# Performance work log

Hardware: AMD Instinct MI355X
Metric: run time of the kernel (lower is better)

The kernel has to match this reference:

```python
import jax, jax.numpy as jnp
import numpy as np

B = 131072
D_IN = 385          # 384-d embedding + 1 correctness feature
D_H = 192           # both trunk layers resolve to max(.,192)=192 per source
Q = 1000            # number of questions
C = 16              # classes per head (uniform padding of per-question heads)


def setup_inputs() -> dict:
    key = jax.random.key(0)
    ks = jax.random.split(key, 9)
    x = jax.random.normal(ks[0], (B, D_IN), dtype=jnp.float32)
    question_ids = jax.random.randint(ks[1], (B,), 0, Q, dtype=jnp.int32)
    is_correct = jax.random.randint(ks[2], (B,), 0, 2, dtype=jnp.int32)
    W1 = jax.random.normal(ks[3], (D_IN, D_H), dtype=jnp.float32) * 0.05
    b1 = jnp.zeros((D_H,), dtype=jnp.float32)
    W2 = jax.random.normal(ks[4], (D_H, D_H), dtype=jnp.float32) * 0.05
    b2 = jnp.zeros((D_H,), dtype=jnp.float32)
    # Head bank: slots [0,Q) = false heads, [Q,2Q) = true heads.
    W_heads = jax.random.normal(ks[5], (2 * Q, C, D_H), dtype=jnp.float32) * 0.05
    b_heads = jax.random.normal(ks[6], (2 * Q, C), dtype=jnp.float32) * 0.05
    return {"x": x, "question_ids": question_ids, "is_correct": is_correct,
            "W1": W1, "b1": b1, "W2": W2, "b2": b2,
            "W_heads": W_heads, "b_heads": b_heads}


def reference(x, question_ids, is_correct, W1, b1, W2, b2, W_heads, b_heads):
    # Shared trunk (eval mode: dropout = identity)
    h = jax.nn.relu(x @ W1 + b1)            # [B, 192]
    feat = jax.nn.relu(h @ W2 + b2)         # [B, 192]
    # Hard routing: pick true or false head for this question.
    Qn = W_heads.shape[0] // 2
    idx = question_ids + is_correct * Qn    # [B]
    Wq = W_heads[idx]                       # [B, C, 192] gather (memory-bound)
    bq = b_heads[idx]                       # [B, C]
    logits = jnp.einsum('bcd,bd->bc', Wq, feat) + bq  # per-sample routed linear
    return logits
```

## Files before the change

### kernel.cpp

```cpp
#include <hip/hip_runtime.h>
#include <hip/hip_bf16.h>
#include <stdint.h>
#include <stddef.h>


typedef short s8v __attribute__((ext_vector_type(8)));
typedef float f4v __attribute__((ext_vector_type(4)));
typedef float f4a __attribute__((ext_vector_type(4), aligned(4)));

typedef const void __attribute__((address_space(1))) *gas1_t;
typedef void __attribute__((address_space(3))) *las3_t;

namespace {
constexpr int kDin = 385;
constexpr int kDh  = 192;
constexpr int kQ   = 1000;
constexpr int kC   = 16;
constexpr int BM   = 64;
constexpr int NT   = 512;
constexpr int NK1  = 13;
constexpr int NK2  = 6;
constexpr int CHUNK = 12 * 64 * 8;
constexpr int H2   = 200;

constexpr size_t WS_W1   = 0;
constexpr size_t WS_W2   = 163840;
constexpr size_t WS_HIST = 245760;
constexpr size_t WS_CUR  = 253952;
constexpr size_t WS_PERM = 262144;

constexpr size_t WB_FEAT = 0;
constexpr size_t WB_W1   = 50331648;
constexpr size_t WB_W2   = WB_W1 + 159744;
constexpr size_t WB_HIST = WB_W2 + 73728;
constexpr size_t WB_CUR  = WB_HIST + 8192;
constexpr size_t WB_PERM = WB_CUR + 8192;
constexpr size_t WB_NEED = WB_PERM + 524288;
constexpr size_t WS_SANE_MAX = (1ull << 36);
}

__device__ __forceinline__ unsigned short f2bf(float f) {
  unsigned int u = __float_as_uint(f);
  u = u + 0x7fffu + ((u >> 16) & 1u);
  return (unsigned short)(u >> 16);
}

__device__ __forceinline__ unsigned int pk2(float lo, float hi) {
  union { __hip_bfloat162 h2; unsigned int u; } cv;
  cv.h2 = __float22bfloat162_rn(make_float2(lo, hi));
  return cv.u;
}

union s8u { s8v s; unsigned int u[4]; };

__device__ __forceinline__ void swz_one(const float* W, int K, int i,
                                        unsigned short* out) {
  int k = i / kDh;
  int c = i - k * kDh;
  float v = (k < K) ? W[(size_t)k * kDh + c] : 0.f;
  int oi = (k >> 5) * CHUNK + (((c >> 4) * 64 + ((k >> 3) & 3) * 16 + (c & 15)) << 3)
         + (k & 7);
  out[oi] = f2bf(v);
}

__global__ void combo_prep(const int* __restrict__ qid, const int* __restrict__ isc,
                           int B, int nbH,
                           const float* __restrict__ W1, const float* __restrict__ W2,
                           int* __restrict__ hist,
                           unsigned short* __restrict__ W1sw,
                           unsigned short* __restrict__ W2sw) {
  int bid = blockIdx.x;
  if (bid < nbH) {
    int i = bid * 256 + threadIdx.x;
    if (i < B) atomicAdd(&hist[qid[i] + isc[i] * kQ], 1);
  } else if (bid < nbH + 312) {
    swz_one(W1, kDin, (bid - nbH) * 256 + threadIdx.x, W1sw);
  } else {
    swz_one(W2, kDh, (bid - nbH - 312) * 256 + threadIdx.x, W2sw);
  }
}

__global__ __launch_bounds__(256)
void scatter2(const int* __restrict__ qid, const int* __restrict__ isc, int B,
              const int* __restrict__ hist, int* __restrict__ rank_ctr,
              int* __restrict__ perm) {
  __shared__ int sh[2048];
  __shared__ int ssum[256];
  int t = threadIdx.x;
  int4 a = ((const int4*)hist)[t * 2];
  int4 b = ((const int4*)hist)[t * 2 + 1];
  int s1 = a.x + a.y, s2 = s1 + a.z, s3 = s2 + a.w;
  int s4 = s3 + b.x, s5 = s4 + b.y, s6 = s5 + b.z, s7 = s6 + b.w;
  ssum[t] = s7;
  __syncthreads();
  #pragma unroll
  for (int d = 1; d < 256; d <<= 1) {
    int xv = (t >= d) ? ssum[t - d] : 0;
    __syncthreads();
    ssum[t] += xv;
    __syncthreads();
  }
  int base = ssum[t] - s7;
  sh[t * 8 + 0] = base;
  sh[t * 8 + 1] = base + a.x;
  sh[t * 8 + 2] = base + s1;
  sh[t * 8 + 3] = base + s2;
  sh[t * 8 + 4] = base + s3;
  sh[t * 8 + 5] = base + s4;
  sh[t * 8 + 6] = base + s5;
  sh[t * 8 + 7] = base + s6;
  __syncthreads();
  int i = blockIdx.x * 256 + t;
  if (i < B) {
    int h = qid[i] + isc[i] * kQ;
    int pos = sh[h] + atomicAdd(&rank_ctr[h], 1);
    perm[pos] = i;
  }
}

__global__ __launch_bounds__(NT, 8)
void trunk_k(const float* __restrict__ x,
             const float* __restrict__ b1,
             const float* __restrict__ b2,
             const unsigned short* __restrict__ W1sw,
             const unsigned short* __restrict__ W2sw,
             unsigned short* __restrict__ featG) {
  __shared__ __align__(16) unsigned short hS[BM * H2];
  __shared__ __align__(16) unsigned short bS[CHUNK];

  const int tid  = threadIdx.x;
  const int lane = tid & 63, wid = tid >> 6;
  const int m = lane & 15, quad = lane >> 4;
  const int rh = wid >> 1, ch = wid & 1;
  const int row0 = blockIdx.x * BM;

  {
    const char* g = (const char*)W1sw + (size_t)tid * 16;
    char* l = (char*)bS + ((tid >> 6) << 10);
    __builtin_amdgcn_global_load_lds((gas1_t)g, (las3_t)l, 16, 0, 0);
    if (tid < 256)
      __builtin_amdgcn_global_load_lds((gas1_t)(g + 8192), (las3_t)(l + 8192),
                                       16, 0, 0);
  }

  const float* px = x + (size_t)(row0 + rh * 16 + m) * kDin;

  f4v acc[6];
  #pragma unroll
  for (int t = 0; t < 6; ++t) acc[t] = (f4v){0.f, 0.f, 0.f, 0.f};

  f4a c0 = *(const f4a*)(px + quad * 8);
  f4a c1 = *(const f4a*)(px + quad * 8 + 4);
  float tl = 0.f;
  __syncthreads();

  #pragma unroll
  for (int kk = 0; kk < NK1; ++kk) {
    s8v a;
    if (kk < NK1 - 1) {
      s8u ua;
      ua.u[0] = pk2(c0[0], c0[1]); ua.u[1] = pk2(c0[2], c0[3]);
      ua.u[2] = pk2(c1[0], c1[1]); ua.u[3] = pk2(c1[2], c1[3]);
      a = ua.s;
    } else {
      a = (s8v){0,0,0,0,0,0,0,0};
      a[0] = (short)f2bf(tl);
    }

    #pragma unroll
    for (int t = 0; t < 6; ++t) {
      s8v b = *(const s8v*)&bS[((ch * 6 + t) * 64 + lane) * 8];
      acc[t] = __builtin_amdgcn_mfma_f32_16x16x32_bf16(a, b, acc[t], 0, 0, 0);
    }
    __syncthreads();

    {
      const unsigned short* np = (kk < NK1 - 1)
          ? W1sw + (size_t)(kk + 1) * CHUNK : W2sw;
      const char* g = (const char*)np + (size_t)tid * 16;
      char* l = (char*)bS + ((tid >> 6) << 10);
      __builtin_amdgcn_global_load_lds((gas1_t)g, (las3_t)l, 16, 0, 0);
      if (tid < 256)
        __builtin_amdgcn_global_load_lds((gas1_t)(g + 8192), (las3_t)(l + 8192),
                                         16, 0, 0);
    }
    if (kk < NK1 - 2) {
      c0 = *(const f4a*)(px + (kk + 1) * 32 + quad * 8);
      c1 = *(const f4a*)(px + (kk + 1) * 32 + quad * 8 + 4);
    } else if (kk == NK1 - 2) {
      tl = (quad == 0) ? px[384] : 0.f;
    }
    if (kk == NK1 - 1) {
      #pragma unroll
      for (int t = 0; t < 6; ++t) {
        int c = ch * 96 + t * 16 + m;
        float bb = b1[c];
        #pragma unroll
        for (int r4 = 0; r4 < 4; ++r4) {
          int r = rh * 16 + quad * 4 + r4;
          float v0 = acc[t][r4] + bb;
          hS[r * H2 + c] = f2bf(v0 > 0.f ? v0 : 0.f);
          acc[t][r4] = 0.f;
        }
      }
    }
    __syncthreads();
  }

  const int ar0 = (rh * 16 + m) * H2;
  #pragma unroll
  for (int k2 = 0; k2 < NK2; ++k2) {
    s8v a = *(const s8v*)&hS[ar0 + k2 * 32 + quad * 8];
    #pragma unroll
    for (int t = 0; t < 6; ++t) {
      s8v b = *(const s8v*)&bS[((ch * 6 + t) * 64 + lane) * 8];
      acc[t] = __builtin_amdgcn_mfma_f32_16x16x32_bf16(a, b, acc[t], 0, 0, 0);
    }
    __syncthreads();
    if (k2 < NK2 - 1) {
      const char* g = (const char*)(W2sw + (size_t)(k2 + 1) * CHUNK)
                    + (size_t)tid * 16;
      char* l = (char*)bS + ((tid >> 6) << 10);
      __builtin_amdgcn_global_load_lds((gas1_t)g, (las3_t)l, 16, 0, 0);
      if (tid < 256)
        __builtin_amdgcn_global_load_lds((gas1_t)(g + 8192), (las3_t)(l + 8192),
                                         16, 0, 0);
    } else {
      #pragma unroll
      for (int t = 0; t < 6; ++t) {
        int c = ch * 96 + t * 16 + m;
        float bb = b2[c];
        #pragma unroll
        for (int r4 = 0; r4 < 4; ++r4) {
          int r = rh * 16 + quad * 4 + r4;
          float v0 = acc[t][r4] + bb;
          hS[r * H2 + c] = f2bf(v0 > 0.f ? v0 : 0.f);
        }
      }
    }
    __syncthreads();
  }

  #pragma unroll
  for (int j = 0; j < 3; ++j) {
    int e = tid + j * NT;
    int row = e / 24, c8 = e - row * 24;
    *(s8v*)&featG[(size_t)(row0 + row) * kDh + c8 * 8] =
        *(const s8v*)&hS[row * H2 + c8 * 8];
  }
}

__global__ __launch_bounds__(NT, 8)
void head_k(const int* __restrict__ qid, const int* __restrict__ isc,
            const float* __restrict__ Wh, const float* __restrict__ bh,
            const unsigned short* __restrict__ featG,
            const int* __restrict__ perm, float* __restrict__ out) {
  __shared__ int permS[BM];
  __shared__ int idxS[BM];

  const int tid  = threadIdx.x;
  const int lane = tid & 63, wid = tid >> 6;
  const int m = lane & 15, quad = lane >> 4;
  const int rh = wid >> 1, ch = wid & 1;
  const int row0 = blockIdx.x * BM;

  if (tid < BM) {
    int p = perm[row0 + tid];
    permS[tid] = p;
    idxS[tid] = qid[p] + isc[p] * kQ;
  }
  __syncthreads();

  const int w16 = rh * 16;
  const unsigned short* fp = featG + (size_t)permS[w16 + m] * kDh + quad * 8;
  s8v f[6];
  #pragma unroll
  for (int kk = 0; kk < 6; ++kk) f[kk] = *(const s8v*)(fp + kk * 32);

  const int hm = idxS[w16 + m];
  const s8v zf = (s8v){0,0,0,0,0,0,0,0};
  unsigned rem = 0xFFFFu;
  int runIdx = 0;
  while (rem) {
    int r0 = (int)__builtin_ctz(rem);
    int h = idxS[w16 + r0];
    unsigned long long bal = __ballot(hm == h);
    unsigned mask16 = (unsigned)(bal & 0xFFFFu);
    rem &= ~mask16;
    if ((runIdx & 1) == ch) {
      bool valid = (hm == h);
      const float* wq = Wh + ((size_t)h * kC + m) * kDh + quad * 8;
      f4v acch = (f4v){0.f, 0.f, 0.f, 0.f};
      #pragma unroll
      for (int kk = 0; kk < 6; ++kk) {
        float4 wlo = *(const float4*)(wq + kk * 32);
        float4 whi = *(const float4*)(wq + kk * 32 + 4);
        s8u ub;
        ub.u[0] = pk2(wlo.x, wlo.y);
        ub.u[1] = pk2(wlo.z, wlo.w);
        ub.u[2] = pk2(whi.x, whi.y);
        ub.u[3] = pk2(whi.z, whi.w);
        s8v afr = valid ? f[kk] : zf;
        acch = __builtin_amdgcn_mfma_f32_16x16x32_bf16(afr, ub.s, acch, 0, 0, 0);
      }
      float bhv = bh[(size_t)h * kC + m];
      #pragma unroll
      for (int reg = 0; reg < 4; ++reg) {
        int r = quad * 4 + reg;
        if ((mask16 >> r) & 1u)
          out[(size_t)permS[w16 + r] * kC + m] = acch[reg] + bhv;
      }
    }
    runIdx++;
  }
}

__global__ __launch_bounds__(NT, 8)
void fused_qmlp8(const float* __restrict__ x,
                 const int*   __restrict__ qid,
                 const int*   __restrict__ isc,
                 const float* __restrict__ b1,
                 const float* __restrict__ b2,
                 const float* __restrict__ Wh,
                 const float* __restrict__ bh,
                 const unsigned short* __restrict__ W1sw,
                 const unsigned short* __restrict__ W2sw,
                 const int*   __restrict__ perm,
                 float* __restrict__ out) {
  __shared__ __align__(16) unsigned short hS[BM * H2];
  __shared__ __align__(16) unsigned short bS[CHUNK];
  __shared__ int permS[BM];
  __shared__ int idxS[BM];

  const int tid  = threadIdx.x;
  const int lane = tid & 63, wid = tid >> 6;
  const int m = lane & 15, quad = lane >> 4;
  const int rh = wid >> 1, ch = wid & 1;
  const int row0 = blockIdx.x * BM;

  {
    const char* g = (const char*)W1sw + (size_t)tid * 16;
    char* l = (char*)bS + ((tid >> 6) << 10);
    __builtin_amdgcn_global_load_lds((gas1_t)g, (las3_t)l, 16, 0, 0);
    if (tid < 256)
      __builtin_amdgcn_global_load_lds((gas1_t)(g + 8192), (las3_t)(l + 8192),
                                       16, 0, 0);
  }
  if (tid < BM) {
    int p = perm[row0 + tid];
    permS[tid] = p;
    idxS[tid] = qid[p] + isc[p] * kQ;
  }
  __syncthreads();

  const float* px = x + (size_t)permS[rh * 16 + m] * kDin;

  f4v acc[6];
  #pragma unroll
  for (int t = 0; t < 6; ++t) acc[t] = (f4v){0.f, 0.f, 0.f, 0.f};

  f4a c0 = *(const f4a*)(px + quad * 8);
  f4a c1 = *(const f4a*)(px + quad * 8 + 4);
  float tl = 0.f;

  #pragma unroll
  for (int kk = 0; kk < NK1; ++kk) {
    s8v a;
    if (kk < NK1 - 1) {
      s8u ua;
      ua.u[0] = pk2(c0[0], c0[1]); ua.u[1] = pk2(c0[2], c0[3]);
      ua.u[2] = pk2(c1[0], c1[1]); ua.u[3] = pk2(c1[2], c1[3]);
      a = ua.s;
    } else {
      a = (s8v){0,0,0,0,0,0,0,0};
      a[0] = (short)f2bf(tl);
    }

    #pragma unroll
    for (int t = 0; t < 6; ++t) {
      s8v b = *(const s8v*)&bS[((ch * 6 + t) * 64 + lane) * 8];
      acc[t] = __builtin_amdgcn_mfma_f32_16x16x32_bf16(a, b, acc[t], 0, 0, 0);
    }
    __syncthreads();

    {
      const unsigned short* np = (kk < NK1 - 1)
          ? W1sw + (size_t)(kk + 1) * CHUNK : W2sw;
      const char* g = (const char*)np + (size_t)tid * 16;
      char* l = (char*)bS + ((tid >> 6) << 10);
      __builtin_amdgcn_global_load_lds((gas1_t)g, (las3_t)l, 16, 0, 0);
      if (tid < 256)
        __builtin_amdgcn_global_load_lds((gas1_t)(g + 8192), (las3_t)(l + 8192),
                                         16, 0, 0);
    }
    if (kk < NK1 - 2) {
      c0 = *(const f4a*)(px + (kk + 1) * 32 + quad * 8);
      c1 = *(const f4a*)(px + (kk + 1) * 32 + quad * 8 + 4);
    } else if (kk == NK1 - 2) {
      tl = (quad == 0) ? px[384] : 0.f;
    }
    if (kk == NK1 - 1) {
      #pragma unroll
      for (int t = 0; t < 6; ++t) {
        int c = ch * 96 + t * 16 + m;
        float bb = b1[c];
        #pragma unroll
        for (int r4 = 0; r4 < 4; ++r4) {
          int r = rh * 16 + quad * 4 + r4;
          float v0 = acc[t][r4] + bb;
          hS[r * H2 + c] = f2bf(v0 > 0.f ? v0 : 0.f);
          acc[t][r4] = 0.f;
        }
      }
    }
    __syncthreads();
  }

  const int ar0 = (rh * 16 + m) * H2;
  #pragma unroll
  for (int k2 = 0; k2 < NK2; ++k2) {
    s8v a = *(const s8v*)&hS[ar0 + k2 * 32 + quad * 8];
    #pragma unroll
    for (int t = 0; t < 6; ++t) {
      s8v b = *(const s8v*)&bS[((ch * 6 + t) * 64 + lane) * 8];
      acc[t] = __builtin_amdgcn_mfma_f32_16x16x32_bf16(a, b, acc[t], 0, 0, 0);
    }
    __syncthreads();
    if (k2 < NK2 - 1) {
      const char* g = (const char*)(W2sw + (size_t)(k2 + 1) * CHUNK)
                    + (size_t)tid * 16;
      char* l = (char*)bS + ((tid >> 6) << 10);
      __builtin_amdgcn_global_load_lds((gas1_t)g, (las3_t)l, 16, 0, 0);
      if (tid < 256)
        __builtin_amdgcn_global_load_lds((gas1_t)(g + 8192), (las3_t)(l + 8192),
                                         16, 0, 0);
    } else {
      #pragma unroll
      for (int t = 0; t < 6; ++t) {
        int c = ch * 96 + t * 16 + m;
        float bb = b2[c];
        #pragma unroll
        for (int r4 = 0; r4 < 4; ++r4) {
          int r = rh * 16 + quad * 4 + r4;
          float v0 = acc[t][r4] + bb;
          hS[r * H2 + c] = f2bf(v0 > 0.f ? v0 : 0.f);
        }
      }
    }
    __syncthreads();
  }

  {
    const int w16 = rh * 16;
    const int hm = idxS[w16 + m];
    unsigned rem = 0xFFFFu;
    int runIdx = 0;
    while (rem) {
      int r0 = (int)__builtin_ctz(rem);
      int h = idxS[w16 + r0];
      unsigned long long bal = __ballot(hm == h);
      unsigned mask16 = (unsigned)(bal & 0xFFFFu);
      rem &= ~mask16;
      if ((runIdx & 1) == ch) {
        const float* wq = Wh + ((size_t)h * kC + m) * kDh + quad * 8;
        f4v acch = (f4v){0.f, 0.f, 0.f, 0.f};
        #pragma unroll
        for (int kk = 0; kk < 6; ++kk) {
          float4 wlo = *(const float4*)(wq + kk * 32);
          float4 whi = *(const float4*)(wq + kk * 32 + 4);
          s8u ub;
          ub.u[0] = pk2(wlo.x, wlo.y);
          ub.u[1] = pk2(wlo.z, wlo.w);
          ub.u[2] = pk2(whi.x, whi.y);
          ub.u[3] = pk2(whi.z, whi.w);
          s8v afr = *(const s8v*)&hS[(w16 + m) * H2 + kk * 32 + quad * 8];
          if (hm != h) afr = (s8v){0,0,0,0,0,0,0,0};
          acch = __builtin_amdgcn_mfma_f32_16x16x32_bf16(afr, ub.s, acch, 0, 0, 0);
        }
        float bhv = bh[(size_t)h * kC + m];
        #pragma unroll
        for (int reg = 0; reg < 4; ++reg) {
          int r = quad * 4 + reg;
          if ((mask16 >> r) & 1u)
            out[(size_t)permS[w16 + r] * kC + m] = acch[reg] + bhv;
        }
      }
      runIdx++;
    }
  }
}

extern "C" void kernel_launch(void* const* d_in, const int* in_sizes, int n_in,
                              void* d_out, int out_size, void* d_ws, size_t ws_size,
                              hipStream_t stream) {
  const float* x  = (const float*)d_in[0];
  const int*   qd = (const int*)  d_in[1];
  const int*   ic = (const int*)  d_in[2];
  const float* W1 = (const float*)d_in[3];
  const float* b1 = (const float*)d_in[4];
  const float* W2 = (const float*)d_in[5];
  const float* b2 = (const float*)d_in[6];
  const float* Wh = (const float*)d_in[7];
  const float* bh = (const float*)d_in[8];
  float* out = (float*)d_out;

  char* ws = (char*)d_ws;
  int B = in_sizes[1];
  int nbH = (B + 255) / 256;

  const bool big = (d_ws != nullptr) && (ws_size >= WB_NEED)
                 && (ws_size < WS_SANE_MAX);

  if (big) {
    unsigned short* featG = (unsigned short*)(ws + WB_FEAT);
    unsigned short* W1sw  = (unsigned short*)(ws + WB_W1);
    unsigned short* W2sw  = (unsigned short*)(ws + WB_W2);
    int* hist = (int*)(ws + WB_HIST);
    int* rank = (int*)(ws + WB_CUR);
    int* perm = (int*)(ws + WB_PERM);

    hipMemsetAsync(hist, 0, 4096 * sizeof(int), stream);
    combo_prep<<<nbH + 312 + 144, 256, 0, stream>>>(qd, ic, B, nbH, W1, W2,
                                                    hist, W1sw, W2sw);
    scatter2<<<(B + 255) / 256, 256, 0, stream>>>(qd, ic, B, hist, rank, perm);
    trunk_k<<<B / BM, NT, 0, stream>>>(x, b1, b2, W1sw, W2sw, featG);
    head_k<<<B / BM, NT, 0, stream>>>(qd, ic, Wh, bh, featG, perm, out);
  } else {
    unsigned short* W1sw = (unsigned short*)(ws + WS_W1);
    unsigned short* W2sw = (unsigned short*)(ws + WS_W2);
    int* hist = (int*)(ws + WS_HIST);
    int* rank = (int*)(ws + WS_CUR);
    int* perm = (int*)(ws + WS_PERM);

    hipMemsetAsync(hist, 0, 4096 * sizeof(int), stream);
    combo_prep<<<nbH + 312 + 144, 256, 0, stream>>>(qd, ic, B, nbH, W1, W2,
                                                    hist, W1sw, W2sw);
    scatter2<<<(B + 255) / 256, 256, 0, stream>>>(qd, ic, B, hist, rank, perm);
    fused_qmlp8<<<B / BM, NT, 0, stream>>>(x, qd, ic, b1, b2, Wh, bh,
                                           W1sw, W2sw, perm, out);
  }
}
```

Before: 419.6 us.

## Double-buffer weight chunks and widen trunk tile to 128 rows per block

The trunk kernel now processes 128 rows per block, with each wave owning 16 full rows across all 192 output columns instead of splitting columns between two waves. Weight chunks are double-buffered in LDS, so the next chunk is prefetched before the MFMAs on the current one, cutting the two barriers per k-step to one. The intent is to halve weight reloads per row and overlap global-to-LDS copies with compute. The cost is more LDS and accumulator registers per block, with occupancy lowered to 4 blocks per CU.

```diff
diff --git a/kernel.cpp b/kernel.cpp
--- a/kernel.cpp
+++ b/kernel.cpp
@@ -17,6 +17,7 @@
 constexpr int kQ   = 1000;
 constexpr int kC   = 16;
 constexpr int BM   = 64;
+constexpr int BM2  = 128;
 constexpr int NT   = 512;
 constexpr int NK1  = 13;
 constexpr int NK2  = 6;
@@ -118,46 +119,60 @@
   }
 }
 
-__global__ __launch_bounds__(NT, 8)
-void trunk_k(const float* __restrict__ x,
-             const float* __restrict__ b1,
-             const float* __restrict__ b2,
-             const unsigned short* __restrict__ W1sw,
-             const unsigned short* __restrict__ W2sw,
-             unsigned short* __restrict__ featG) {
-  __shared__ __align__(16) unsigned short hS[BM * H2];
-  __shared__ __align__(16) unsigned short bS[CHUNK];
+__device__ __forceinline__ void stage2(const unsigned short* gsrc,
+                                       unsigned short* lbase, int tid) {
+  const char* g = (const char*)gsrc + (size_t)tid * 16;
+  char* l = (char*)lbase + ((tid >> 6) << 10);
+  __builtin_amdgcn_global_load_lds((gas1_t)g, (las3_t)l, 16, 0, 0);
+  if (tid < 256)
+    __builtin_amdgcn_global_load_lds((gas1_t)(g + 8192), (las3_t)(l + 8192),
+                                     16, 0, 0);
+}
+
+__global__ __launch_bounds__(NT, 4)
+void trunk_k2(const float* __restrict__ x,
+              const float* __restrict__ b1,
+              const float* __restrict__ b2,
+              const unsigned short* __restrict__ W1sw,
+              const unsigned short* __restrict__ W2sw,
+              unsigned short* __restrict__ featG) {
+  __shared__ __align__(16) unsigned short hS[BM2 * H2];
+  __shared__ __align__(16) unsigned short bS[2 * CHUNK];
 
   const int tid  = threadIdx.x;
   const int lane = tid & 63, wid = tid >> 6;
   const int m = lane & 15, quad = lane >> 4;
-  const int rh = wid >> 1, ch = wid & 1;
-  const int row0 = blockIdx.x * BM;
-
-  {
-    const char* g = (const char*)W1sw + (size_t)tid * 16;
-    char* l = (char*)bS + ((tid >> 6) << 10);
-    __builtin_amdgcn_global_load_lds((gas1_t)g, (las3_t)l, 16, 0, 0);
-    if (tid < 256)
-      __builtin_amdgcn_global_load_lds((gas1_t)(g + 8192), (las3_t)(l + 8192),
-                                       16, 0, 0);
-  }
-
-  const float* px = x + (size_t)(row0 + rh * 16 + m) * kDin;
-
-  f4v acc[6];
-  #pragma unroll
-  for (int t = 0; t < 6; ++t) acc[t] = (f4v){0.f, 0.f, 0.f, 0.f};
-
+  const int w16 = wid * 16;
+  const int row0 = blockIdx.x * BM2;
+
+  const float* px = x + (size_t)(row0 + w16 + m) * kDin;
+
+  stage2(W1sw, bS, tid);
   f4a c0 = *(const f4a*)(px + quad * 8);
   f4a c1 = *(const f4a*)(px + quad * 8 + 4);
   float tl = 0.f;
+
+  f4v acc[12];
+  #pragma unroll
+  for (int t = 0; t < 12; ++t) acc[t] = (f4v){0.f, 0.f, 0.f, 0.f};
   __syncthreads();
 
   #pragma unroll
-  for (int kk = 0; kk < NK1; ++kk) {
+  for (int g = 0; g < NK1; ++g) {
+    const unsigned short* np = (g < NK1 - 1)
+        ? W1sw + (size_t)(g + 1) * CHUNK : W2sw;
+    stage2(np, bS + ((g + 1) & 1) * CHUNK, tid);
+
+    f4a n0, n1;
+    if (g < NK1 - 2) {
+      n0 = *(const f4a*)(px + (g + 1) * 32 + quad * 8);
+      n1 = *(const f4a*)(px + (g + 1) * 32 + quad * 8 + 4);
+    } else if (g == NK1 - 2) {
+      tl = (quad == 0) ? px[384] : 0.f;
+    }
+
     s8v a;
-    if (kk < NK1 - 1) {
+    if (g < NK1 - 1) {
       s8u ua;
       ua.u[0] = pk2(c0[0], c0[1]); ua.u[1] = pk2(c0[2], c0[3]);
       ua.u[2] = pk2(c1[0], c1[1]); ua.u[3] = pk2(c1[2], c1[3]);
@@ -167,37 +182,21 @@
       a[0] = (short)f2bf(tl);
     }
 
+    const unsigned short* bB = bS + (g & 1) * CHUNK;
     #pragma unroll
-    for (int t = 0; t < 6; ++t) {
-      s8v b = *(const s8v*)&bS[((ch * 6 + t) * 64 + lane) * 8];
+    for (int t = 0; t < 12; ++t) {
+      s8v b = *(const s8v*)&bB[(t * 64 + lane) * 8];
       acc[t] = __builtin_amdgcn_mfma_f32_16x16x32_bf16(a, b, acc[t], 0, 0, 0);
     }
-    __syncthreads();
-
-    {
-      const unsigned short* np = (kk < NK1 - 1)
-          ? W1sw + (size_t)(kk + 1) * CHUNK : W2sw;
-      const char* g = (const char*)np + (size_t)tid * 16;
-      char* l = (char*)bS + ((tid >> 6) << 10);
-      __builtin_amdgcn_global_load_lds((gas1_t)g, (las3_t)l, 16, 0, 0);
-      if (tid < 256)
-        __builtin_amdgcn_global_load_lds((gas1_t)(g + 8192), (las3_t)(l + 8192),
-                                         16, 0, 0);
-    }
-    if (kk < NK1 - 2) {
-      c0 = *(const f4a*)(px + (kk + 1) * 32 + quad * 8);
-      c1 = *(const f4a*)(px + (kk + 1) * 32 + quad * 8 + 4);
-    } else if (kk == NK1 - 2) {
-      tl = (quad == 0) ? px[384] : 0.f;
-    }
-    if (kk == NK1 - 1) {
+
+    if (g == NK1 - 1) {
       #pragma unroll
-      for (int t = 0; t < 6; ++t) {
-        int c = ch * 96 + t * 16 + m;
+      for (int t = 0; t < 12; ++t) {
+        int c = t * 16 + m;
         float bb = b1[c];
         #pragma unroll
         for (int r4 = 0; r4 < 4; ++r4) {
-          int r = rh * 16 + quad * 4 + r4;
+          int r = w16 + quad * 4 + r4;
           float v0 = acc[t][r4] + bb;
           hS[r * H2 + c] = f2bf(v0 > 0.f ? v0 : 0.f);
           acc[t][r4] = 0.f;
@@ -205,44 +204,41 @@
       }
     }
     __syncthreads();
-  }
-
-  const int ar0 = (rh * 16 + m) * H2;
+    if (g < NK1 - 2) { c0 = n0; c1 = n1; }
+  }
+
   #pragma unroll
   for (int k2 = 0; k2 < NK2; ++k2) {
-    s8v a = *(const s8v*)&hS[ar0 + k2 * 32 + quad * 8];
+    const int g = NK1 + k2;
+    if (k2 < NK2 - 1)
+      stage2(W2sw + (size_t)(k2 + 1) * CHUNK,
+             bS + ((g + 1) & 1) * CHUNK, tid);
+
+    s8v a = *(const s8v*)&hS[(w16 + m) * H2 + k2 * 32 + quad * 8];
+    const unsigned short* bB = bS + (g & 1) * CHUNK;
     #pragma unroll
-    for (int t = 0; t < 6; ++t) {
-      s8v b = *(const s8v*)&bS[((ch * 6 + t) * 64 + lane) * 8];
+    for (int t = 0; t < 12; ++t) {
+      s8v b = *(const s8v*)&bB[(t * 64 + lane) * 8];
       acc[t] = __builtin_amdgcn_mfma_f32_16x16x32_bf16(a, b, acc[t], 0, 0, 0);
     }
-    __syncthreads();
-    if (k2 < NK2 - 1) {
-      const char* g = (const char*)(W2sw + (size_t)(k2 + 1) * CHUNK)
-                    + (size_t)tid * 16;
-      char* l = (char*)bS + ((tid >> 6) << 10);
-      __builtin_amdgcn_global_load_lds((gas1_t)g, (las3_t)l, 16, 0, 0);
-      if (tid < 256)
-        __builtin_amdgcn_global_load_lds((gas1_t)(g + 8192), (las3_t)(l + 8192),
-                                         16, 0, 0);
-    } else {
-      #pragma unroll
-      for (int t = 0; t < 6; ++t) {
-        int c = ch * 96 + t * 16 + m;
-        float bb = b2[c];
-        #pragma unroll
-        for (int r4 = 0; r4 < 4; ++r4) {
-          int r = rh * 16 + quad * 4 + r4;
-          float v0 = acc[t][r4] + bb;
-          hS[r * H2 + c] = f2bf(v0 > 0.f ? v0 : 0.f);
-        }
-      }
-    }
-    __syncthreads();
-  }
-
-  #pragma unroll
-  for (int j = 0; j < 3; ++j) {
+    if (k2 < NK2 - 1) __syncthreads();
+  }
+
+  #pragma unroll
+  for (int t = 0; t < 12; ++t) {
+    int c = t * 16 + m;
+    float bb = b2[c];
+    #pragma unroll
+    for (int r4 = 0; r4 < 4; ++r4) {
+      int r = w16 + quad * 4 + r4;
+      float v0 = acc[t][r4] + bb;
+      hS[r * H2 + c] = f2bf(v0 > 0.f ? v0 : 0.f);
+    }
+  }
+  __syncthreads();
+
+  #pragma unroll
+  for (int j = 0; j < 6; ++j) {
     int e = tid + j * NT;
     int row = e / 24, c8 = e - row * 24;
     *(s8v*)&featG[(size_t)(row0 + row) * kDh + c8 * 8] =
@@ -523,7 +519,7 @@
     combo_prep<<<nbH + 312 + 144, 256, 0, stream>>>(qd, ic, B, nbH, W1, W2,
                                                     hist, W1sw, W2sw);
     scatter2<<<(B + 255) / 256, 256, 0, stream>>>(qd, ic, B, hist, rank, perm);
-    trunk_k<<<B / BM, NT, 0, stream>>>(x, b1, b2, W1sw, W2sw, featG);
+    trunk_k2<<<B / BM2, NT, 0, stream>>>(x, b1, b2, W1sw, W2sw, featG);
     head_k<<<B / BM, NT, 0, stream>>>(qd, ic, Wh, bh, featG, perm, out);
   } else {
     unsigned short* W1sw = (unsigned short*)(ws + WS_W1);
```

New measurement: 400.2 us. 4.6% less time.
